# Performance work log

Hardware: AMD Instinct MI355X
Metric: run time of the kernel (lower is better)

## Reference

```python
import jax, jax.numpy as jnp
import numpy as np

N = 50000      # nodes
E = 1600000    # edges (avg degree 32)
C_IN = 128
C_H = 128
C_OUT = 10
G = 512        # number of graphs in the batch


def setup_inputs() -> dict:
    key = jax.random.key(0)
    ks = jax.random.split(key, 16)
    x = jax.random.normal(ks[0], (N, C_IN), dtype=jnp.float32)
    edge_index = jax.random.randint(ks[1], (2, E), 0, N, dtype=jnp.int64)
    batch = jnp.sort(jax.random.randint(ks[2], (N,), 0, G, dtype=jnp.int64))

    def lin(k, fan_in, fan_out):
        lim = 1.0 / np.sqrt(fan_in)
        return jax.random.uniform(k, (fan_in, fan_out), jnp.float32, -lim, lim)

    return {
        "x": x, "edge_index": edge_index, "batch": batch,
        # conv1: c_in -> c_hidden
        "Wr1": lin(ks[3], C_IN, C_H), "br1": jnp.zeros((C_H,), jnp.float32),
        "Wo1": lin(ks[4], C_IN, C_H),
        # conv2: c_hidden -> 2*c_hidden
        "Wr2": lin(ks[5], C_H, 2 * C_H), "br2": jnp.zeros((2 * C_H,), jnp.float32),
        "Wo2": lin(ks[6], C_H, 2 * C_H),
        # conv3: 2*c_hidden -> c_hidden
        "Wr3": lin(ks[7], 2 * C_H, C_H), "br3": jnp.zeros((C_H,), jnp.float32),
        "Wo3": lin(ks[8], 2 * C_H, C_H),
        # head
        "W1": lin(ks[9], C_H, 4 * C_OUT), "b1": jnp.zeros((4 * C_OUT,), jnp.float32),
        "W2": lin(ks[10], 4 * C_OUT, C_OUT), "b2": jnp.zeros((C_OUT,), jnp.float32),
    }


def _graph_conv(x, src, dst, Wr, br, Wo):
    # PyG GraphConv: lin_rel(sum_{j in N(i)} x_j) + lin_root(x_i)
    agg = jax.ops.segment_sum(x[src], dst, num_segments=N)  # [N, F_in]
    return agg @ Wr + br + x @ Wo


def reference(x, edge_index, batch, Wr1, br1, Wo1, Wr2, br2, Wo2,
              Wr3, br3, Wo3, W1, b1, W2, b2):
    src, dst = edge_index[0], edge_index[1]
    h = jax.nn.relu(_graph_conv(x, src, dst, Wr1, br1, Wo1))
    h = jax.nn.relu(_graph_conv(h, src, dst, Wr2, br2, Wo2))
    h = _graph_conv(h, src, dst, Wr3, br3, Wo3)
    # global mean pool over graphs
    sums = jax.ops.segment_sum(h, batch, num_segments=G)            # [G, C_H]
    cnts = jax.ops.segment_sum(jnp.ones((N,), h.dtype), batch, num_segments=G)
    pooled = sums / jnp.maximum(cnts, 1.0)[:, None]
    # dropout is identity in eval mode
    out = pooled @ W1 + b1
    out = out @ W2 + b2
    return out
```

## Files before the change

### kernel.cpp

```cpp
#include <hip/hip_runtime.h>
#include <hip/hip_bf16.h>
#include <cstddef>

#define NN 50000
#define EE 1600000
#define GG 512
#define NB 196
#define BSTRIDE 16384
#define BCAP 10240
#define XBLKS 6250
#define SCBLKS 782

typedef unsigned int u32;
typedef unsigned short u16;
typedef __attribute__((ext_vector_type(8))) short frag_ab;
typedef __attribute__((ext_vector_type(4))) float frag_cd;

__device__ __forceinline__ void gl_lds16(const void* g, void* l) {
    __builtin_amdgcn_global_load_lds(
        (const __attribute__((address_space(1))) u32*)g,
        (__attribute__((address_space(3))) u32*)l, 16, 0, 0);
}
__device__ __forceinline__ float b2f_lo(u32 v) { return __uint_as_float(v << 16); }
__device__ __forceinline__ float b2f_hi(u32 v) { return __uint_as_float(v & 0xffff0000u); }
__device__ __forceinline__ float b2f(u32 v, int odd) { return odd ? b2f_hi(v) : b2f_lo(v); }
__device__ __forceinline__ u16 f2b(float x) {
    __hip_bfloat16 h = __float2bfloat16(x);
    return *(u16*)&h;
}
__device__ __forceinline__ u32 pack2(float lo, float hi) {
    return ((u32)f2b(hi) << 16) | f2b(lo);
}
__device__ __forceinline__ void acc2(float2& a, u32 v) {
    a.x += b2f_lo(v);
    a.y += b2f_hi(v);
}



__global__ __launch_bounds__(256) void bscatter_prep_kernel(
    const int* __restrict__ ei, int* __restrict__ bcnt, u32* __restrict__ pairs,
    const float* __restrict__ x, u16* __restrict__ ax,
    const float* __restrict__ Wr1, const float* __restrict__ Wo1,
    const float* __restrict__ Wr2, const float* __restrict__ Wo2,
    const float* __restrict__ Wr3, const float* __restrict__ Wo3,
    const float* __restrict__ br3,
    u16* __restrict__ BT1, u16* __restrict__ BT2, u16* __restrict__ BT3,
    float* __restrict__ bias3) {
    __shared__ int lcnt[NB];
    __shared__ int lbase[NB];
    __shared__ unsigned short lpos[2048];
    int bid = blockIdx.x, t = threadIdx.x;
    if (bid < SCBLKS) {
        int e0 = bid * 2048;
        u32 pk[8];
        int bk[8];
        for (int i = t; i < NB; i += 256) lcnt[i] = 0;
        __syncthreads();
#pragma unroll
        for (int i = 0; i < 8; ++i) {
            int e = e0 + i * 256 + t;
            if (e < EE) {
                int dst = ei[EE + e], src = ei[e];
                int b = dst >> 8;
                bk[i] = b;
                pk[i] = ((u32)src << 8) | (u32)(dst & 255);
                lpos[i * 256 + t] = (unsigned short)atomicAdd(&lcnt[b], 1);
            } else bk[i] = -1;
        }
        __syncthreads();
        for (int i = t; i < NB; i += 256) lbase[i] = atomicAdd(&bcnt[i], lcnt[i]);
        __syncthreads();
#pragma unroll
        for (int i = 0; i < 8; ++i) {
            if (bk[i] >= 0) {
                int pos = lbase[bk[i]] + (int)lpos[i * 256 + t];
                pairs[(size_t)bk[i] * BSTRIDE + pos] = pk[i];
            }
        }
    } else if (bid < SCBLKS + XBLKS) {
        int idx = (bid - SCBLKS) * 256 + t;
        int row = idx >> 5, q = idx & 31;
        float4 v = *(const float4*)(x + (size_t)row * 128 + q * 4);
        *(u32*)(ax + (size_t)row * 256 + 128 + q * 4) = pack2(v.x, v.y);
        *(u32*)(ax + (size_t)row * 256 + 128 + q * 4 + 2) = pack2(v.z, v.w);
    } else {
        int m = bid - SCBLKS - XBLKS;
        int k = t;
        BT2[m * 256 + k] = f2b(k < 128 ? Wr2[k * 256 + m] : Wo2[(k - 128) * 256 + m]);
        BT3[m * 256 + k] = f2b(m < 128 ? Wr3[k * 128 + m] : Wo3[k * 128 + (m - 128)]);
        if (m < 128)
            BT1[m * 256 + k] = f2b(k < 128 ? Wr1[k * 128 + m] : Wo1[(k - 128) * 128 + m]);
        if (k == 0) bias3[m] = (m < 128) ? 0.f : br3[m - 128];
    }
}


__global__ __launch_bounds__(512) void bfill_kernel(const u32* __restrict__ pairs,
                                                    const int* __restrict__ bcnt,
                                                    int* __restrict__ ofs,
                                                    u16* __restrict__ srcl) {
    __shared__ int sc[256];
    __shared__ int cnts[256];
    __shared__ int lcnt[256];
    __shared__ int lcur[256];
    __shared__ int lbuf[BCAP];
    int b = blockIdx.x, t = threadIdx.x;
    if (t < 256) {
        int c = (t < NB) ? bcnt[t] : 0;
        cnts[t] = c;
        sc[t] = c;
        lcnt[t] = 0;
    }
    __syncthreads();
    for (int off = 1; off < 256; off <<= 1) {
        int v = (t >= off && t < 256) ? sc[t - off] : 0;
        __syncthreads();
        if (t < 256) sc[t] += v;
        __syncthreads();
    }
    int base = sc[b] - cnts[b];
    int span = cnts[b];
    const u32* pp = pairs + (size_t)b * BSTRIDE;
    for (int j = t; j < span; j += 512) atomicAdd(&lcnt[pp[j] & 255u], 1);
    __syncthreads();
    int nc = 0;
    if (t < 256) {
        nc = lcnt[t];
        sc[t] = nc;
    }
    __syncthreads();
    for (int off = 1; off < 256; off <<= 1) {
        int v = (t >= off && t < 256) ? sc[t - off] : 0;
        __syncthreads();
        if (t < 256) sc[t] += v;
        __syncthreads();
    }
    if (t < 256) {
        int excl = sc[t] - nc;
        int node = b * 256 + t;
        if (node < NN) ofs[node] = base + excl;
        lcur[t] = excl;
    }
    if (b == 0 && t == 256) ofs[NN] = EE;
    __syncthreads();
    for (int j = t; j < span; j += 512) {
        u32 p = pp[j];
        int pos = atomicAdd(&lcur[p & 255u], 1);
        int src = (int)(p >> 8);
        if (pos < BCAP) lbuf[pos] = src;
        else srcl[base + pos] = (u16)src;
    }
    __syncthreads();
    int lim = span < BCAP ? span : BCAP;
    for (int j = t; j < lim; j += 512) srcl[base + j] = (u16)lbuf[j];
}


__global__ __launch_bounds__(256) void pull_bf_kernel(const u32* __restrict__ Xu,
                                                      const int* __restrict__ ofs,
                                                      const u16* __restrict__ srcl,
                                                      u32* __restrict__ outu) {
    int node = (blockIdx.x * 256 + threadIdx.x) >> 6;
    int lane = threadIdx.x & 63;
    int q = lane >> 4, l = lane & 15;
    int lo = ofs[node], hi = ofs[node + 1];
    float2 a0 = {0.f, 0.f}, a1 = {0.f, 0.f}, a2 = {0.f, 0.f}, a3 = {0.f, 0.f};
    int j = lo;
    for (; j + 15 < hi; j += 16) {
        int s0 = srcl[j + q], s1 = srcl[j + 4 + q];
        int s2 = srcl[j + 8 + q], s3 = srcl[j + 12 + q];
        uint4 v0 = *(const uint4*)(Xu + (size_t)s0 * 128 + l * 4);
        uint4 v1 = *(const uint4*)(Xu + (size_t)s1 * 128 + l * 4);
        uint4 v2 = *(const uint4*)(Xu + (size_t)s2 * 128 + l * 4);
        uint4 v3 = *(const uint4*)(Xu + (size_t)s3 * 128 + l * 4);
        acc2(a0, v0.x); acc2(a1, v0.y); acc2(a2, v0.z); acc2(a3, v0.w);
        acc2(a0, v1.x); acc2(a1, v1.y); acc2(a2, v1.z); acc2(a3, v1.w);
        acc2(a0, v2.x); acc2(a1, v2.y); acc2(a2, v2.z); acc2(a3, v2.w);
        acc2(a0, v3.x); acc2(a1, v3.y); acc2(a2, v3.z); acc2(a3, v3.w);
    }
    for (; j + 3 < hi; j += 4) {
        int s = srcl[j + q];
        uint4 v = *(const uint4*)(Xu + (size_t)s * 128 + l * 4);
        acc2(a0, v.x); acc2(a1, v.y); acc2(a2, v.z); acc2(a3, v.w);
    }
    if (j + q < hi) {
        int s = srcl[j + q];
        uint4 v = *(const uint4*)(Xu + (size_t)s * 128 + l * 4);
        acc2(a0, v.x); acc2(a1, v.y); acc2(a2, v.z); acc2(a3, v.w);
    }
    float acc[8] = {a0.x, a0.y, a1.x, a1.y, a2.x, a2.y, a3.x, a3.y};
#pragma unroll
    for (int i = 0; i < 8; ++i) {
        acc[i] += __shfl_xor(acc[i], 16, 64);
        acc[i] += __shfl_xor(acc[i], 32, 64);
    }
    if (q == 0) {
        uint4 r;
        r.x = pack2(acc[0], acc[1]);
        r.y = pack2(acc[2], acc[3]);
        r.z = pack2(acc[4], acc[5]);
        r.w = pack2(acc[6], acc[7]);
        *(uint4*)(outu + (size_t)node * 128 + l * 4) = r;
    }
}


__global__ __launch_bounds__(256, 2) void gemm_bf_kernel(
    const u16* __restrict__ A, const u16* __restrict__ BT,
    const float* __restrict__ bias, u16* __restrict__ C,
    int ldc, int coloff, int relu) {
    __shared__ alignas(16) u16 As[128 * 32];
    __shared__ alignas(16) u16 Bs[128 * 32];
    const int t = threadIdx.x;
    const int lane = t & 63, wid = t >> 6;
    const int quad = lane >> 4, l16 = lane & 15;
    const int wm = wid >> 1, wn = wid & 1;
    const int row0 = blockIdx.y * 128, c0 = blockIdx.x * 128;

    frag_cd acc[4][4];
#pragma unroll
    for (int i = 0; i < 4; ++i)
#pragma unroll
        for (int j = 0; j < 4; ++j) acc[i][j] = (frag_cd)0.f;

    const int ca = t, cb = t + 256;
    const int ra = ca >> 2, oa = (ca & 3) * 8;
    const int rb = cb >> 2, ob = (cb & 3) * 8;
    const int garow = min(row0 + ra, NN - 1);
    const int gbrow = min(row0 + rb, NN - 1);
    const size_t gA1 = (size_t)garow * 256 + oa;
    const size_t gA2 = (size_t)gbrow * 256 + ob;
    const size_t gB1 = (size_t)(c0 + ra) * 256 + oa;
    const size_t gB2 = (size_t)(c0 + rb) * 256 + ob;

    for (int kk = 0; kk < 256; kk += 32) {
        __syncthreads();
        gl_lds16(A + gA1 + kk, &As[ca * 8]);
        gl_lds16(A + gA2 + kk, &As[cb * 8]);
        gl_lds16(BT + gB1 + kk, &Bs[ca * 8]);
        gl_lds16(BT + gB2 + kk, &Bs[cb * 8]);
        __syncthreads();

        frag_ab a[4], b[4];
#pragma unroll
        for (int mt = 0; mt < 4; ++mt)
            a[mt] = *(const frag_ab*)&As[(wm * 64 + mt * 16 + l16) * 32 + quad * 8];
#pragma unroll
        for (int nt = 0; nt < 4; ++nt)
            b[nt] = *(const frag_ab*)&Bs[(wn * 64 + nt * 16 + l16) * 32 + quad * 8];
#pragma unroll
        for (int mt = 0; mt < 4; ++mt)
#pragma unroll
            for (int nt = 0; nt < 4; ++nt)
                acc[mt][nt] = __builtin_amdgcn_mfma_f32_16x16x32_bf16(
                    a[mt], b[nt], acc[mt][nt], 0, 0, 0);
    }

#pragma unroll
    for (int nt = 0; nt < 4; ++nt) {
        int col = c0 + wn * 64 + nt * 16 + l16;
        float bv = bias[col];
#pragma unroll
        for (int mt = 0; mt < 4; ++mt) {
#pragma unroll
            for (int r = 0; r < 4; ++r) {
                int row = row0 + wm * 64 + mt * 16 + quad * 4 + r;
                if (row < NN) {
                    float v = acc[mt][nt][r] + bv;
                    if (relu) v = fmaxf(v, 0.f);
                    C[(size_t)row * ldc + coloff + col] = f2b(v);
                }
            }
        }
    }
}


__global__ __launch_bounds__(256, 2) void gemm23_kernel(
    const u16* __restrict__ A, const u16* __restrict__ BT2,
    const float* __restrict__ br2, const u16* __restrict__ BT3,
    const float* __restrict__ bias3, u16* __restrict__ C) {
    __shared__ alignas(16) u16 As[128 * 32];
    __shared__ alignas(16) u16 Bs[128 * 32];
    __shared__ alignas(16) u16 Hs[128 * 256];
    const int t = threadIdx.x;
    const int lane = t & 63, wid = t >> 6;
    const int quad = lane >> 4, l16 = lane & 15;
    const int wm = wid >> 1, wn = wid & 1;
    const int row0 = blockIdx.x * 128;

    const int ca = t, cb = t + 256;
    const int ra = ca >> 2, oa = (ca & 3) * 8;
    const int rb = cb >> 2, ob = (cb & 3) * 8;
    const int garow = min(row0 + ra, NN - 1);
    const int gbrow = min(row0 + rb, NN - 1);
    const size_t gA1 = (size_t)garow * 256 + oa;
    const size_t gA2 = (size_t)gbrow * 256 + ob;

    for (int nb = 0; nb < 2; ++nb) {
        const int c0 = nb * 128;
        frag_cd acc[4][4];
#pragma unroll
        for (int i = 0; i < 4; ++i)
#pragma unroll
            for (int j = 0; j < 4; ++j) acc[i][j] = (frag_cd)0.f;

        for (int kk = 0; kk < 256; kk += 32) {
            __syncthreads();
            gl_lds16(A + gA1 + kk, &As[ca * 8]);
            gl_lds16(A + gA2 + kk, &As[cb * 8]);
            gl_lds16(BT2 + (size_t)(c0 + ra) * 256 + kk + oa, &Bs[ca * 8]);
            gl_lds16(BT2 + (size_t)(c0 + rb) * 256 + kk + ob, &Bs[cb * 8]);
            __syncthreads();

            frag_ab a[4], b[4];
#pragma unroll
            for (int mt = 0; mt < 4; ++mt)
                a[mt] = *(const frag_ab*)&As[(wm * 64 + mt * 16 + l16) * 32 + quad * 8];
#pragma unroll
            for (int nt = 0; nt < 4; ++nt)
                b[nt] = *(const frag_ab*)&Bs[(wn * 64 + nt * 16 + l16) * 32 + quad * 8];
#pragma unroll
            for (int mt = 0; mt < 4; ++mt)
#pragma unroll
                for (int nt = 0; nt < 4; ++nt)
                    acc[mt][nt] = __builtin_amdgcn_mfma_f32_16x16x32_bf16(
                        a[mt], b[nt], acc[mt][nt], 0, 0, 0);
        }
#pragma unroll
        for (int nt = 0; nt < 4; ++nt) {
            int col = c0 + wn * 64 + nt * 16 + l16;
            float bv = br2[col];
#pragma unroll
            for (int mt = 0; mt < 4; ++mt) {
#pragma unroll
                for (int r = 0; r < 4; ++r) {
                    int lr = wm * 64 + mt * 16 + quad * 4 + r;
                    float v = fmaxf(acc[mt][nt][r] + bv, 0.f);
                    Hs[(lr * 256 + col) ^ ((lr & 7) << 3)] = f2b(v);
                }
            }
        }
    }
    __syncthreads();

    for (int nb = 0; nb < 2; ++nb) {
        const int c0 = nb * 128;
        frag_cd acc[4][4];
#pragma unroll
        for (int i = 0; i < 4; ++i)
#pragma unroll
            for (int j = 0; j < 4; ++j) acc[i][j] = (frag_cd)0.f;

        for (int kk = 0; kk < 256; kk += 32) {
            __syncthreads();
            gl_lds16(BT3 + (size_t)(c0 + ra) * 256 + kk + oa, &Bs[ca * 8]);
            gl_lds16(BT3 + (size_t)(c0 + rb) * 256 + kk + ob, &Bs[cb * 8]);
            __syncthreads();

            frag_ab a[4], b[4];
#pragma unroll
            for (int mt = 0; mt < 4; ++mt) {
                int lr = wm * 64 + mt * 16 + l16;
                a[mt] = *(const frag_ab*)&Hs[(lr * 256 + kk + quad * 8) ^ ((lr & 7) << 3)];
            }
#pragma unroll
            for (int nt = 0; nt < 4; ++nt)
                b[nt] = *(const frag_ab*)&Bs[(wn * 64 + nt * 16 + l16) * 32 + quad * 8];
#pragma unroll
            for (int mt = 0; mt < 4; ++mt)
#pragma unroll
                for (int nt = 0; nt < 4; ++nt)
                    acc[mt][nt] = __builtin_amdgcn_mfma_f32_16x16x32_bf16(
                        a[mt], b[nt], acc[mt][nt], 0, 0, 0);
        }
#pragma unroll
        for (int nt = 0; nt < 4; ++nt) {
            int col = c0 + wn * 64 + nt * 16 + l16;
            float bv = bias3[col];
#pragma unroll
            for (int mt = 0; mt < 4; ++mt) {
#pragma unroll
                for (int r = 0; r < 4; ++r) {
                    int row = row0 + wm * 64 + mt * 16 + quad * 4 + r;
                    if (row < NN) {
                        float v = acc[mt][nt][r] + bv;
                        C[(size_t)row * 256 + col] = f2b(v);
                    }
                }
            }
        }
    }
}


__device__ inline int lower_bound_i(const int* a, int n, int v) {
    int lo = 0, hi = n;
    while (lo < hi) {
        int m = (lo + hi) >> 1;
        if (a[m] < v) lo = m + 1; else hi = m;
    }
    return lo;
}

__global__ __launch_bounds__(1024) void pool3_kernel(
    const u32* __restrict__ Tu, const int* __restrict__ ofs,
    const u16* __restrict__ srcl, const int* __restrict__ batch,
    const float* __restrict__ W1, const float* __restrict__ b1,
    const float* __restrict__ W2, const float* __restrict__ b2,
    float* __restrict__ out) {
    __shared__ float red[16][128];
    __shared__ float po[8][128];
    __shared__ float p[128];
    __shared__ float hid[40];
    int g = blockIdx.x, t = threadIdx.x;
    int w = t >> 6, lane = t & 63;
    int q = lane >> 4, l = lane & 15;
    int n_lo = lower_bound_i(batch, NN, g);
    int n_hi = lower_bound_i(batch, NN, g + 1);
    int glo = ofs[n_lo], ghi = ofs[n_hi];

    float2 a0 = {0.f, 0.f}, a1 = {0.f, 0.f}, a2 = {0.f, 0.f}, a3 = {0.f, 0.f};
    for (int gb = glo + w * 64; gb < ghi; gb += 1024) {
        int nedge = ghi - gb;
        if (nedge > 64) nedge = 64;
        int idx = (lane < nedge) ? (int)srcl[gb + lane] : 0;
        if (nedge == 64) {
            int s0 = __shfl(idx, q, 64);
            int s1 = __shfl(idx, 4 + q, 64);
            int s2 = __shfl(idx, 8 + q, 64);
            int s3 = __shfl(idx, 12 + q, 64);
            uint4 v0 = *(const uint4*)(Tu + (size_t)s0 * 128 + l * 4);
            uint4 v1 = *(const uint4*)(Tu + (size_t)s1 * 128 + l * 4);
            uint4 v2 = *(const uint4*)(Tu + (size_t)s2 * 128 + l * 4);
            uint4 v3 = *(const uint4*)(Tu + (size_t)s3 * 128 + l * 4);
#pragma unroll
            for (int b = 1; b < 4; ++b) {
                int u0 = __shfl(idx, b * 16 + q, 64);
                int u1 = __shfl(idx, b * 16 + 4 + q, 64);
                int u2 = __shfl(idx, b * 16 + 8 + q, 64);
                int u3 = __shfl(idx, b * 16 + 12 + q, 64);
                uint4 w0 = *(const uint4*)(Tu + (size_t)u0 * 128 + l * 4);
                uint4 w1 = *(const uint4*)(Tu + (size_t)u1 * 128 + l * 4);
                uint4 w2 = *(const uint4*)(Tu + (size_t)u2 * 128 + l * 4);
                uint4 w3 = *(const uint4*)(Tu + (size_t)u3 * 128 + l * 4);
                acc2(a0, v0.x); acc2(a1, v0.y); acc2(a2, v0.z); acc2(a3, v0.w);
                acc2(a0, v1.x); acc2(a1, v1.y); acc2(a2, v1.z); acc2(a3, v1.w);
                acc2(a0, v2.x); acc2(a1, v2.y); acc2(a2, v2.z); acc2(a3, v2.w);
                acc2(a0, v3.x); acc2(a1, v3.y); acc2(a2, v3.z); acc2(a3, v3.w);
                v0 = w0; v1 = w1; v2 = w2; v3 = w3;
            }
            acc2(a0, v0.x); acc2(a1, v0.y); acc2(a2, v0.z); acc2(a3, v0.w);
            acc2(a0, v1.x); acc2(a1, v1.y); acc2(a2, v1.z); acc2(a3, v1.w);
            acc2(a0, v2.x); acc2(a1, v2.y); acc2(a2, v2.z); acc2(a3, v2.w);
            acc2(a0, v3.x); acc2(a1, v3.y); acc2(a2, v3.z); acc2(a3, v3.w);
        } else {
#pragma unroll
            for (int b = 0; b < 4; ++b) {
#pragma unroll
                for (int sl = 0; sl < 4; ++sl) {
                    int e = b * 16 + sl * 4 + q;
                    int s = __shfl(idx, e, 64);
                    if (e < nedge) {
                        uint4 v = *(const uint4*)(Tu + (size_t)s * 128 + l * 4);
                        acc2(a0, v.x); acc2(a1, v.y); acc2(a2, v.z); acc2(a3, v.w);
                    }
                }
            }
        }
    }
    float acc[8] = {a0.x, a0.y, a1.x, a1.y, a2.x, a2.y, a3.x, a3.y};
#pragma unroll
    for (int i = 0; i < 8; ++i) {
        acc[i] += __shfl_xor(acc[i], 16, 64);
        acc[i] += __shfl_xor(acc[i], 32, 64);
    }
    if (q == 0) {
#pragma unroll
        for (int i = 0; i < 8; ++i) red[w][l * 8 + i] = acc[i];
    }
    float so = 0.f;
    int ch = t & 127, rg = t >> 7;
    for (int r = n_lo + rg; r < n_hi; r += 8)
        so += b2f(Tu[(size_t)r * 128 + 64 + (ch >> 1)], ch & 1);
    po[rg][ch] = so;
    __syncthreads();
    if (t < 128) {
        float s = 0.f;
#pragma unroll
        for (int k = 0; k < 16; ++k) s += red[k][t];
#pragma unroll
        for (int k = 0; k < 8; ++k) s += po[k][t];
        p[t] = s / fmaxf((float)(n_hi - n_lo), 1.f);
    }
    __syncthreads();
    if (t < 40) {
        float v = b1[t];
        for (int k = 0; k < 128; ++k) v += p[k] * W1[k * 40 + t];
        hid[t] = v;
    }
    __syncthreads();
    if (t < 10) {
        float v = b2[t];
        for (int j = 0; j < 40; ++j) v += hid[j] * W2[j * 10 + t];
        out[g * 10 + t] = v;
    }
}


extern "C" void kernel_launch(void* const* d_in, const int* in_sizes, int n_in,
                              void* d_out, int out_size, void* d_ws, size_t ws_size,
                              hipStream_t stream) {
    const float* x   = (const float*)d_in[0];
    const int* ei    = (const int*)d_in[1];
    const int* batch = (const int*)d_in[2];
    const float* Wr1 = (const float*)d_in[3];
    const float* br1 = (const float*)d_in[4];
    const float* Wo1 = (const float*)d_in[5];
    const float* Wr2 = (const float*)d_in[6];
    const float* br2 = (const float*)d_in[7];
    const float* Wo2 = (const float*)d_in[8];
    const float* Wr3 = (const float*)d_in[9];
    const float* br3 = (const float*)d_in[10];
    const float* Wo3 = (const float*)d_in[11];
    const float* W1  = (const float*)d_in[12];
    const float* b1  = (const float*)d_in[13];
    const float* W2  = (const float*)d_in[14];
    const float* b2  = (const float*)d_in[15];
    float* out = (float*)d_out;

    char* ws = (char*)d_ws;
    size_t off = 0;
    auto alloc = [&](size_t bytes) {
        void* p = ws + off;
        off += (bytes + 255) & ~(size_t)255;
        return p;
    };
    int* ofs      = (int*)alloc((NN + 1) * sizeof(int));
    int* bcnt     = (int*)alloc(256 * sizeof(int));
    u16* srcl     = (u16*)alloc((size_t)EE * 2);
    u16* ax       = (u16*)alloc((size_t)NN * 256 * 2);
    u16* ah1      = (u16*)alloc((size_t)NN * 256 * 2);
    u16* t3o3     = (u16*)alloc((size_t)NN * 256 * 2);
    u16* BT1      = (u16*)alloc(128 * 256 * 2);
    u16* BT2      = (u16*)alloc(256 * 256 * 2);
    u16* BT3      = (u16*)alloc(256 * 256 * 2);
    float* bias3  = (float*)alloc(256 * sizeof(float));
    u32* pairs = (u32*)t3o3;

    hipMemsetAsync(bcnt, 0, 256 * sizeof(int), stream);

    bscatter_prep_kernel<<<SCBLKS + XBLKS + 256, 256, 0, stream>>>(
        ei, bcnt, pairs, x, ax, Wr1, Wo1, Wr2, Wo2, Wr3, Wo3, br3,
        BT1, BT2, BT3, bias3);
    bfill_kernel<<<NB, 512, 0, stream>>>(pairs, bcnt, ofs, srcl);

    pull_bf_kernel<<<NN * 64 / 256, 256, 0, stream>>>((const u32*)ax + 64, ofs, srcl, (u32*)ax);
    gemm_bf_kernel<<<dim3(1, 391), 256, 0, stream>>>(ax, BT1, br1, ah1, 256, 128, 1);
    pull_bf_kernel<<<NN * 64 / 256, 256, 0, stream>>>((const u32*)ah1 + 64, ofs, srcl, (u32*)ah1);
    gemm23_kernel<<<391, 256, 0, stream>>>(ah1, BT2, br2, BT3, bias3, t3o3);

    pool3_kernel<<<GG, 1024, 0, stream>>>((const u32*)t3o3, ofs, srcl, batch,
                                          W1, b1, W2, b2, out);
}
```

Before: 352.1 us.

## Split graph pooling into segmented partial-sum blocks plus separate head kernel

Replaces the one-block-per-graph pooling kernel with 8 smaller blocks per graph. Each block sums a contiguous slice of the graph's edge range and node range into a partial-sum buffer, and a new head kernel reduces the partials and applies the MLP. The graph boundaries are now found once with a binary search in the prep kernel instead of in every pooling block. This is meant to improve load balance and occupancy in the pooling stage, at the cost of an extra kernel launch and a round trip through global memory for the partials.

```diff
diff --git a/kernel.cpp b/kernel.cpp
--- a/kernel.cpp
+++ b/kernel.cpp
@@ -10,6 +10,7 @@
 #define BCAP 10240
 #define XBLKS 6250
 #define SCBLKS 782
+#define PSEG 8
 
 typedef unsigned int u32;
 typedef unsigned short u16;
@@ -34,6 +35,15 @@
 __device__ __forceinline__ void acc2(float2& a, u32 v) {
     a.x += b2f_lo(v);
     a.y += b2f_hi(v);
+}
+
+__device__ inline int lower_bound_i(const int* a, int n, int v) {
+    int lo = 0, hi = n;
+    while (lo < hi) {
+        int m = (lo + hi) >> 1;
+        if (a[m] < v) lo = m + 1; else hi = m;
+    }
+    return lo;
 }
 
 
@@ -46,7 +56,8 @@
     const float* __restrict__ Wr3, const float* __restrict__ Wo3,
     const float* __restrict__ br3,
     u16* __restrict__ BT1, u16* __restrict__ BT2, u16* __restrict__ BT3,
-    float* __restrict__ bias3) {
+    float* __restrict__ bias3, const int* __restrict__ batch,
+    int* __restrict__ gn) {
     __shared__ int lcnt[NB];
     __shared__ int lbase[NB];
     __shared__ unsigned short lpos[2048];
@@ -84,7 +95,7 @@
         float4 v = *(const float4*)(x + (size_t)row * 128 + q * 4);
         *(u32*)(ax + (size_t)row * 256 + 128 + q * 4) = pack2(v.x, v.y);
         *(u32*)(ax + (size_t)row * 256 + 128 + q * 4 + 2) = pack2(v.z, v.w);
-    } else {
+    } else if (bid < SCBLKS + XBLKS + 256) {
         int m = bid - SCBLKS - XBLKS;
         int k = t;
         BT2[m * 256 + k] = f2b(k < 128 ? Wr2[k * 256 + m] : Wo2[(k - 128) * 256 + m]);
@@ -92,6 +103,9 @@
         if (m < 128)
             BT1[m * 256 + k] = f2b(k < 128 ? Wr1[k * 128 + m] : Wo1[(k - 128) * 128 + m]);
         if (k == 0) bias3[m] = (m < 128) ? 0.f : br3[m - 128];
+    } else {
+        int g = (bid - SCBLKS - XBLKS - 256) * 256 + t;
+        if (g <= GG) gn[g] = lower_bound_i(batch, NN, g);
     }
 }
 
@@ -395,105 +409,86 @@
 }
 
 
-__device__ inline int lower_bound_i(const int* a, int n, int v) {
-    int lo = 0, hi = n;
-    while (lo < hi) {
-        int m = (lo + hi) >> 1;
-        if (a[m] < v) lo = m + 1; else hi = m;
-    }
-    return lo;
-}
-
-__global__ __launch_bounds__(1024) void pool3_kernel(
+__global__ __launch_bounds__(256) void pool3_seg_kernel(
     const u32* __restrict__ Tu, const int* __restrict__ ofs,
-    const u16* __restrict__ srcl, const int* __restrict__ batch,
+    const u16* __restrict__ srcl, const int* __restrict__ gn,
+    float* __restrict__ psum) {
+    __shared__ float red[4][128];
+    __shared__ float po[2][128];
+    int gb = blockIdx.x;
+    int g = gb >> 3, s = gb & 7;
+    int t = threadIdx.x;
+    int w = t >> 6, lane = t & 63;
+    int q = lane >> 4, l = lane & 15;
+    int n_lo = gn[g], n_hi = gn[g + 1];
+    int glo = ofs[n_lo], ghi = ofs[n_hi];
+    int len = ghi - glo;
+    int s_lo = glo + (int)(((long long)len * s) >> 3);
+    int s_hi = glo + (int)(((long long)len * (s + 1)) >> 3);
+    int slen = s_hi - s_lo;
+    int wlo = s_lo + ((slen * w) >> 2);
+    int whi = s_lo + ((slen * (w + 1)) >> 2);
+
+    float2 a0 = {0.f, 0.f}, a1 = {0.f, 0.f}, a2 = {0.f, 0.f}, a3 = {0.f, 0.f};
+    int j = wlo;
+    for (; j + 15 < whi; j += 16) {
+        int s0 = srcl[j + q], s1 = srcl[j + 4 + q];
+        int s2 = srcl[j + 8 + q], s3 = srcl[j + 12 + q];
+        uint4 v0 = *(const uint4*)(Tu + (size_t)s0 * 128 + l * 4);
+        uint4 v1 = *(const uint4*)(Tu + (size_t)s1 * 128 + l * 4);
+        uint4 v2 = *(const uint4*)(Tu + (size_t)s2 * 128 + l * 4);
+        uint4 v3 = *(const uint4*)(Tu + (size_t)s3 * 128 + l * 4);
+        acc2(a0, v0.x); acc2(a1, v0.y); acc2(a2, v0.z); acc2(a3, v0.w);
+        acc2(a0, v1.x); acc2(a1, v1.y); acc2(a2, v1.z); acc2(a3, v1.w);
+        acc2(a0, v2.x); acc2(a1, v2.y); acc2(a2, v2.z); acc2(a3, v2.w);
+        acc2(a0, v3.x); acc2(a1, v3.y); acc2(a2, v3.z); acc2(a3, v3.w);
+    }
+    for (; j + 3 < whi; j += 4) {
+        int sv = srcl[j + q];
+        uint4 v = *(const uint4*)(Tu + (size_t)sv * 128 + l * 4);
+        acc2(a0, v.x); acc2(a1, v.y); acc2(a2, v.z); acc2(a3, v.w);
+    }
+    if (j + q < whi) {
+        int sv = srcl[j + q];
+        uint4 v = *(const uint4*)(Tu + (size_t)sv * 128 + l * 4);
+        acc2(a0, v.x); acc2(a1, v.y); acc2(a2, v.z); acc2(a3, v.w);
+    }
+    float acc[8] = {a0.x, a0.y, a1.x, a1.y, a2.x, a2.y, a3.x, a3.y};
+#pragma unroll
+    for (int i = 0; i < 8; ++i) {
+        acc[i] += __shfl_xor(acc[i], 16, 64);
+        acc[i] += __shfl_xor(acc[i], 32, 64);
+    }
+    if (q == 0) {
+#pragma unroll
+        for (int i = 0; i < 8; ++i) red[w][l * 8 + i] = acc[i];
+    }
+    float so = 0.f;
+    int ch = t & 127, rg = t >> 7;
+    for (int r = n_lo + s * 2 + rg; r < n_hi; r += 16)
+        so += b2f(Tu[(size_t)r * 128 + 64 + (ch >> 1)], ch & 1);
+    po[rg][ch] = so;
+    __syncthreads();
+    if (t < 128) {
+        float v = red[0][t] + red[1][t] + red[2][t] + red[3][t] + po[0][t] + po[1][t];
+        psum[((size_t)g * PSEG + s) * 128 + t] = v;
+    }
+}
+
+
+__global__ __launch_bounds__(128) void head_kernel(
+    const float* __restrict__ psum, const int* __restrict__ gn,
     const float* __restrict__ W1, const float* __restrict__ b1,
     const float* __restrict__ W2, const float* __restrict__ b2,
     float* __restrict__ out) {
-    __shared__ float red[16][128];
-    __shared__ float po[8][128];
     __shared__ float p[128];
     __shared__ float hid[40];
     int g = blockIdx.x, t = threadIdx.x;
-    int w = t >> 6, lane = t & 63;
-    int q = lane >> 4, l = lane & 15;
-    int n_lo = lower_bound_i(batch, NN, g);
-    int n_hi = lower_bound_i(batch, NN, g + 1);
-    int glo = ofs[n_lo], ghi = ofs[n_hi];
-
-    float2 a0 = {0.f, 0.f}, a1 = {0.f, 0.f}, a2 = {0.f, 0.f}, a3 = {0.f, 0.f};
-    for (int gb = glo + w * 64; gb < ghi; gb += 1024) {
-        int nedge = ghi - gb;
-        if (nedge > 64) nedge = 64;
-        int idx = (lane < nedge) ? (int)srcl[gb + lane] : 0;
-        if (nedge == 64) {
-            int s0 = __shfl(idx, q, 64);
-            int s1 = __shfl(idx, 4 + q, 64);
-            int s2 = __shfl(idx, 8 + q, 64);
-            int s3 = __shfl(idx, 12 + q, 64);
-            uint4 v0 = *(const uint4*)(Tu + (size_t)s0 * 128 + l * 4);
-            uint4 v1 = *(const uint4*)(Tu + (size_t)s1 * 128 + l * 4);
-            uint4 v2 = *(const uint4*)(Tu + (size_t)s2 * 128 + l * 4);
-            uint4 v3 = *(const uint4*)(Tu + (size_t)s3 * 128 + l * 4);
-#pragma unroll
-            for (int b = 1; b < 4; ++b) {
-                int u0 = __shfl(idx, b * 16 + q, 64);
-                int u1 = __shfl(idx, b * 16 + 4 + q, 64);
-                int u2 = __shfl(idx, b * 16 + 8 + q, 64);
-                int u3 = __shfl(idx, b * 16 + 12 + q, 64);
-                uint4 w0 = *(const uint4*)(Tu + (size_t)u0 * 128 + l * 4);
-                uint4 w1 = *(const uint4*)(Tu + (size_t)u1 * 128 + l * 4);
-                uint4 w2 = *(const uint4*)(Tu + (size_t)u2 * 128 + l * 4);
-                uint4 w3 = *(const uint4*)(Tu + (size_t)u3 * 128 + l * 4);
-                acc2(a0, v0.x); acc2(a1, v0.y); acc2(a2, v0.z); acc2(a3, v0.w);
-                acc2(a0, v1.x); acc2(a1, v1.y); acc2(a2, v1.z); acc2(a3, v1.w);
-                acc2(a0, v2.x); acc2(a1, v2.y); acc2(a2, v2.z); acc2(a3, v2.w);
-                acc2(a0, v3.x); acc2(a1, v3.y); acc2(a2, v3.z); acc2(a3, v3.w);
-                v0 = w0; v1 = w1; v2 = w2; v3 = w3;
-            }
-            acc2(a0, v0.x); acc2(a1, v0.y); acc2(a2, v0.z); acc2(a3, v0.w);
-            acc2(a0, v1.x); acc2(a1, v1.y); acc2(a2, v1.z); acc2(a3, v1.w);
-            acc2(a0, v2.x); acc2(a1, v2.y); acc2(a2, v2.z); acc2(a3, v2.w);
-            acc2(a0, v3.x); acc2(a1, v3.y); acc2(a2, v3.z); acc2(a3, v3.w);
-        } else {
-#pragma unroll
-            for (int b = 0; b < 4; ++b) {
-#pragma unroll
-                for (int sl = 0; sl < 4; ++sl) {
-                    int e = b * 16 + sl * 4 + q;
-                    int s = __shfl(idx, e, 64);
-                    if (e < nedge) {
-                        uint4 v = *(const uint4*)(Tu + (size_t)s * 128 + l * 4);
-                        acc2(a0, v.x); acc2(a1, v.y); acc2(a2, v.z); acc2(a3, v.w);
-                    }
-                }
-            }
-        }
-    }
-    float acc[8] = {a0.x, a0.y, a1.x, a1.y, a2.x, a2.y, a3.x, a3.y};
-#pragma unroll
-    for (int i = 0; i < 8; ++i) {
-        acc[i] += __shfl_xor(acc[i], 16, 64);
-        acc[i] += __shfl_xor(acc[i], 32, 64);
-    }
-    if (q == 0) {
-#pragma unroll
-        for (int i = 0; i < 8; ++i) red[w][l * 8 + i] = acc[i];
-    }
-    float so = 0.f;
-    int ch = t & 127, rg = t >> 7;
-    for (int r = n_lo + rg; r < n_hi; r += 8)
-        so += b2f(Tu[(size_t)r * 128 + 64 + (ch >> 1)], ch & 1);
-    po[rg][ch] = so;
-    __syncthreads();
-    if (t < 128) {
-        float s = 0.f;
-#pragma unroll
-        for (int k = 0; k < 16; ++k) s += red[k][t];
-#pragma unroll
-        for (int k = 0; k < 8; ++k) s += po[k][t];
-        p[t] = s / fmaxf((float)(n_hi - n_lo), 1.f);
-    }
+    int cnt = gn[g + 1] - gn[g];
+    float sv = 0.f;
+#pragma unroll
+    for (int k = 0; k < PSEG; ++k) sv += psum[((size_t)g * PSEG + k) * 128 + t];
+    p[t] = sv / fmaxf((float)cnt, 1.f);
     __syncthreads();
     if (t < 40) {
         float v = b1[t];
@@ -539,10 +534,12 @@
     };
     int* ofs      = (int*)alloc((NN + 1) * sizeof(int));
     int* bcnt     = (int*)alloc(256 * sizeof(int));
+    int* gn       = (int*)alloc((GG + 1) * sizeof(int));
     u16* srcl     = (u16*)alloc((size_t)EE * 2);
     u16* ax       = (u16*)alloc((size_t)NN * 256 * 2);
     u16* ah1      = (u16*)alloc((size_t)NN * 256 * 2);
     u16* t3o3     = (u16*)alloc((size_t)NN * 256 * 2);
+    float* psum   = (float*)alloc((size_t)GG * PSEG * 128 * sizeof(float));
     u16* BT1      = (u16*)alloc(128 * 256 * 2);
     u16* BT2      = (u16*)alloc(256 * 256 * 2);
     u16* BT3      = (u16*)alloc(256 * 256 * 2);
@@ -551,9 +548,9 @@
 
     hipMemsetAsync(bcnt, 0, 256 * sizeof(int), stream);
 
-    bscatter_prep_kernel<<<SCBLKS + XBLKS + 256, 256, 0, stream>>>(
+    bscatter_prep_kernel<<<SCBLKS + XBLKS + 256 + 3, 256, 0, stream>>>(
         ei, bcnt, pairs, x, ax, Wr1, Wo1, Wr2, Wo2, Wr3, Wo3, br3,
-        BT1, BT2, BT3, bias3);
+        BT1, BT2, BT3, bias3, batch, gn);
     bfill_kernel<<<NB, 512, 0, stream>>>(pairs, bcnt, ofs, srcl);
 
     pull_bf_kernel<<<NN * 64 / 256, 256, 0, stream>>>((const u32*)ax + 64, ofs, srcl, (u32*)ax);
@@ -561,6 +558,6 @@
     pull_bf_kernel<<<NN * 64 / 256, 256, 0, stream>>>((const u32*)ah1 + 64, ofs, srcl, (u32*)ah1);
     gemm23_kernel<<<391, 256, 0, stream>>>(ah1, BT2, br2, BT3, bias3, t3o3);
 
-    pool3_kernel<<<GG, 1024, 0, stream>>>((const u32*)t3o3, ofs, srcl, batch,
-                                          W1, b1, W2, b2, out);
-}
+    pool3_seg_kernel<<<GG * PSEG, 256, 0, stream>>>((const u32*)t3o3, ofs, srcl, gn, psum);
+    head_kernel<<<GG, 128, 0, stream>>>(psum, gn, W1, b1, W2, b2, out);
+}
```

New measurement: 344.2 us. 1.02x faster.
